# Kernel tuning notes

Measured on AMD Instinct MI355X. Metric: run time of the kernel, lower is better.

Reference implementation:

```python
import jax, jax.numpy as jnp
import numpy as np

C = 256
GROUPS = 8
EPS = 1e-5

def group_norm(x, gamma, beta):
    # x: [B, C, L]
    B, Cc, L = x.shape
    xg = x.reshape(B, GROUPS, Cc // GROUPS, L)
    mu = xg.mean(axis=(2, 3), keepdims=True)
    var = xg.var(axis=(2, 3), keepdims=True)
    xn = (xg - mu) / jnp.sqrt(var + EPS)
    xn = xn.reshape(B, Cc, L)
    return xn * gamma[None, :, None] + beta[None, :, None]

def conv1x1(x, W, b):
    # W: [Cout, Cin], x: [B, Cin, L]
    return jnp.einsum('oc,bcl->bol', W, x) + b[None, :, None]

def setup_inputs() -> dict:
    key = jax.random.key(0)
    ks = jax.random.split(key, 11)
    s = 1.0 / np.sqrt(C)
    inp = {
        'x': jax.random.normal(ks[0], (8, C, 2048), dtype=jnp.float32),
        'gamma': jnp.ones((C,), jnp.float32),
        'beta': jnp.zeros((C,), jnp.float32),
        'Wq': jax.random.uniform(ks[1], (C, C), jnp.float32, -s, s),
        'bq': jax.random.uniform(ks[2], (C,), jnp.float32, -s, s),
        'Wk': jax.random.uniform(ks[3], (C, C), jnp.float32, -s, s),
        'bk': jax.random.uniform(ks[4], (C,), jnp.float32, -s, s),
        'Wv': jax.random.uniform(ks[5], (C, C), jnp.float32, -s, s),
        'bv': jax.random.uniform(ks[6], (C,), jnp.float32, -s, s),
        'Wo': jax.random.uniform(ks[7], (C, C), jnp.float32, -s, s),
        'bo': jax.random.uniform(ks[8], (C,), jnp.float32, -s, s),
    }
    return inp

def reference(x, gamma, beta, Wq, bq, Wk, bk, Wv, bv, Wo, bo):
    h = group_norm(x, gamma, beta)
    q = conv1x1(h, Wq, bq)  # [B, C, L]
    k = conv1x1(h, Wk, bk)
    v = conv1x1(h, Wv, bv)
    scale = x.shape[1] ** (-0.5)
    attn = jnp.einsum('bci,bcj->bij', q, k) * scale  # [B, L, L]
    attn = jax.nn.softmax(attn, axis=-1)
    out = jnp.einsum('bij,bcj->bci', attn, v)  # [B, C, L]
    out = conv1x1(out, Wo, bo)
    return x + out
```

## Files before the change

kernel.cpp:

```cpp
#include <hip/hip_runtime.h>
#include <hip/hip_bf16.h>
#include <stddef.h>

#define NB 8
#define NC 256
#define NL 2048

typedef __attribute__((ext_vector_type(8))) short s16x8;
typedef __attribute__((ext_vector_type(4))) float f32x4;

__device__ __forceinline__ short f2bs(float x){
  __hip_bfloat16 h = __float2bfloat16(x);
  return __builtin_bit_cast(short, h);
}
__device__ __forceinline__ float bs2f(short x){
  unsigned u = ((unsigned)(unsigned short)x) << 16;
  return __builtin_bit_cast(float, u);
}

#define MFMA16(a,b,c) __builtin_amdgcn_mfma_f32_16x16x32_bf16((a),(b),(c),0,0,0)

__global__ __launch_bounds__(256) void k_stats_prep(const float* __restrict__ x, float* __restrict__ gpart,
                                                    const float* __restrict__ wq, const float* __restrict__ wk,
                                                    const float* __restrict__ wv, const float* __restrict__ wo,
                                                    short* __restrict__ wout){
  const int t = threadIdx.x;
  if (blockIdx.x >= 512){
    int idx = (blockIdx.x - 512) * 256 + t;
    int which = idx >> 16;
    int off = idx & 65535;
    const float* src = (which == 0) ? wq : (which == 1) ? wk : (which == 2) ? wv : wo;
    float sc = (which == 0) ? 0.0625f : 1.0f;
    wout[idx] = f2bs(src[off] * sc);
    return;
  }
  const int idx = blockIdx.x;
  const float4* base = (const float4*)(x + (size_t)idx * 8192);
  float s = 0.f, ss = 0.f;
  for (int i = t; i < 2048; i += 256){
    float4 v = base[i];
    s  += v.x + v.y + v.z + v.w;
    ss += v.x*v.x + v.y*v.y + v.z*v.z + v.w*v.w;
  }
  #pragma unroll
  for (int m = 32; m; m >>= 1){ s += __shfl_down(s, m); ss += __shfl_down(ss, m); }
  __shared__ float red[8];
  if ((t & 63) == 0){ red[t >> 6] = s; red[4 + (t >> 6)] = ss; }
  __syncthreads();
  if (t == 0){
    gpart[idx * 2 + 0] = red[0] + red[1] + red[2] + red[3];
    gpart[idx * 2 + 1] = red[4] + red[5] + red[6] + red[7];
  }
}

__global__ __launch_bounds__(256) void k_gapply(const float* __restrict__ x, const float* __restrict__ gamma,
                                                const float* __restrict__ beta, const float* __restrict__ gpart,
                                                short* __restrict__ ht){
  const int idx = blockIdx.x;
  const int bg = idx >> 3, lt8 = idx & 7;
  const int b = bg >> 3, g = bg & 7;
  float S = 0.f, SS = 0.f;
  #pragma unroll
  for (int s2 = 0; s2 < 8; ++s2){ S += gpart[(bg * 8 + s2) * 2]; SS += gpart[(bg * 8 + s2) * 2 + 1]; }
  const float mu = S * (1.f / 65536.f);
  const float var = SS * (1.f / 65536.f) - mu * mu;
  const float rstd = rsqrtf(var + 1e-5f);
  const float* xg = x + (size_t)bg * 65536;
  const int t = threadIdx.x;
  const int cc = t >> 3, lch = t & 7;
  const int c = g * 32 + cc;
  const float gsc = gamma[c] * rstd;
  const float gbi = beta[c] - mu * gsc;
  __shared__ short tile[64 * 33];
  const int ll_s = t & 63, cg = t >> 6;
  for (int lt = 0; lt < 4; ++lt){
    const int l0 = lt8 * 256 + lt * 64;
    const float4* rp = (const float4*)(xg + (size_t)cc * NL + l0 + lch * 8);
    float4 a = rp[0], bv = rp[1];
    float vals[8] = {a.x, a.y, a.z, a.w, bv.x, bv.y, bv.z, bv.w};
    short o[8];
    #pragma unroll
    for (int e = 0; e < 8; ++e) o[e] = f2bs(vals[e] * gsc + gbi);
    __syncthreads();
    #pragma unroll
    for (int e = 0; e < 8; ++e) tile[(lch * 8 + e) * 33 + cc] = o[e];
    __syncthreads();
    s16x8 pk;
    #pragma unroll
    for (int e = 0; e < 8; ++e) pk[e] = tile[ll_s * 33 + cg * 8 + e];
    *(s16x8*)(ht + ((size_t)(b * NL) + l0 + ll_s) * NC + g * 32 + cg * 8) = pk;
  }
}

__global__ __launch_bounds__(256) void k_conv_qkv(const short* __restrict__ ht, const short* __restrict__ wbf,
                                                  const float* __restrict__ bq, const float* __restrict__ bk,
                                                  const float* __restrict__ bv,
                                                  short* __restrict__ qt, short* __restrict__ kt,
                                                  short* __restrict__ vt){
  const int z = blockIdx.z;
  const int b = z & 7, which = z >> 3;
  const int lane = threadIdx.x & 63, wid = threadIdx.x >> 6;
  const int wr = wid >> 1, wc = wid & 1;
  const int kgrp = (lane >> 4) * 8;
  const short* aptr;
  const short* bptr;
  int m0, n0;
  if (which < 2){
    m0 = blockIdx.y * 128 + wr * 64;
    n0 = blockIdx.x * 64 + wc * 32;
    aptr = ht + ((size_t)(b * NL) + m0 + (lane & 15)) * NC + kgrp;
    bptr = wbf + (which ? 65536 : 0) + (size_t)(n0 + (lane & 15)) * NC + kgrp;
  } else {
    const int idx = blockIdx.y * 4 + blockIdx.x;
    m0 = (idx >> 5) * 128 + wr * 64;
    n0 = (idx & 31) * 64 + wc * 32;
    aptr = wbf + 2 * 65536 + (size_t)(m0 + (lane & 15)) * NC + kgrp;
    bptr = ht + ((size_t)(b * NL) + n0 + (lane & 15)) * NC + kgrp;
  }
  f32x4 acc[4][2];
  #pragma unroll
  for (int i = 0; i < 4; ++i){
    #pragma unroll
    for (int j = 0; j < 2; ++j){ f32x4 z2 = {0.f,0.f,0.f,0.f}; acc[i][j] = z2; }
  }
  #pragma unroll 2
  for (int kk = 0; kk < 256; kk += 32){
    s16x8 af[4], bfr[2];
    #pragma unroll
    for (int mf = 0; mf < 4; ++mf) af[mf] = *(const s16x8*)(aptr + (size_t)(mf * 16) * NC + kk);
    #pragma unroll
    for (int nf = 0; nf < 2; ++nf) bfr[nf] = *(const s16x8*)(bptr + (size_t)(nf * 16) * NC + kk);
    #pragma unroll
    for (int mf = 0; mf < 4; ++mf)
      #pragma unroll
      for (int nf = 0; nf < 2; ++nf)
        acc[mf][nf] = MFMA16(af[mf], bfr[nf], acc[mf][nf]);
  }
  if (which < 2){
    const float* bias = which ? bk : bq;
    const float bsc = which ? 1.0f : 0.0625f;
    short* outp = which ? kt : qt;
    #pragma unroll
    for (int nf = 0; nf < 2; ++nf){
      const int oc = n0 + nf * 16 + (lane & 15);
      const float bb = bias[oc] * bsc;
      #pragma unroll
      for (int mf = 0; mf < 4; ++mf){
        #pragma unroll
        for (int r = 0; r < 4; ++r){
          const int lr = m0 + mf * 16 + (lane >> 4) * 4 + r;
          outp[((size_t)(b * NL) + lr) * NC + oc] = f2bs(acc[mf][nf][r] + bb);
        }
      }
    }
  } else {
    #pragma unroll
    for (int mf = 0; mf < 4; ++mf){
      #pragma unroll
      for (int r = 0; r < 4; ++r){
        const int orow = m0 + mf * 16 + (lane >> 4) * 4 + r;
        const float bb = bv[orow];
        #pragma unroll
        for (int nf = 0; nf < 2; ++nf){
          const int lcol = n0 + nf * 16 + (lane & 15);
          vt[((size_t)(b * NC) + orow) * NL + lcol] = f2bs(acc[mf][nf][r] + bb);
        }
      }
    }
  }
}

__global__ __launch_bounds__(256, 2) void k_flash(const short* __restrict__ qt, const short* __restrict__ kt,
                                                  const short* __restrict__ v, short* __restrict__ po,
                                                  float* __restrict__ ml){
  const int flat = blockIdx.x;
  const int b = flat & 7;
  const int rest = flat >> 3;
  const int h = rest & 1;
  const int i0 = (rest >> 1) * 64;
  const int lane = threadIdx.x & 63, wid = threadIdx.x >> 6;
  __shared__ short k_lds[64 * 256];
  __shared__ short v_lds[256 * 64];
  __shared__ short plds[4][1024];
  short* pl = plds[wid];
  const int arow = lane & 15, kg = lane >> 4;

  const short* qp = qt + ((size_t)(b * NL) + i0 + wid * 16 + arow) * NC + kg * 8;
  s16x8 qf[8];
  #pragma unroll
  for (int kc = 0; kc < 8; ++kc) qf[kc] = *(const s16x8*)(qp + kc * 32);

  f32x4 oacc[16];
  #pragma unroll
  for (int i = 0; i < 16; ++i){ f32x4 z = {0.f,0.f,0.f,0.f}; oacc[i] = z; }
  float m_r[4], l_r[4];
  #pragma unroll
  for (int r = 0; r < 4; ++r){ m_r[r] = -3.0e38f; l_r[r] = 0.f; }

  auto STAGE_K = [&](int jt){
    const int j0 = jt * 64;
    #pragma unroll
    for (int t = 0; t < 8; ++t){
      const int i = wid * 8 + t;
      const int r = 2 * i + (lane >> 5);
      const int wb = (lane & 31) * 16;
      const short* src = kt + ((size_t)(b * NL) + j0 + r) * NC + ((wb ^ ((r & 15) << 4)) >> 1);
      __builtin_amdgcn_global_load_lds((const __attribute__((address_space(1))) void*)src,
                                       (__attribute__((address_space(3))) void*)&k_lds[i * 512], 16, 0, 0);
    }
  };
  auto STAGE_V = [&](int jt){
    const int j0 = jt * 64;
    #pragma unroll
    for (int t = 0; t < 8; ++t){
      const int i = wid * 8 + t;
      const int rc = 8 * i + (lane >> 3);
      const int wb = (lane & 7) * 16;
      const short* src = v + ((size_t)(b * NC) + rc) * NL + j0 + ((wb ^ ((rc & 7) << 4)) >> 1);
      __builtin_amdgcn_global_load_lds((const __attribute__((address_space(1))) void*)src,
                                       (__attribute__((address_space(3))) void*)&v_lds[i * 512], 16, 0, 0);
    }
  };

  const int jb0 = h * 16, jend = jb0 + 16;
  STAGE_K(jb0);
  STAGE_V(jb0);
  asm volatile("s_waitcnt vmcnt(0)" ::: "memory");
  __builtin_amdgcn_s_barrier();
  __builtin_amdgcn_sched_barrier(0);

  for (int jt = jb0; jt < jend; ++jt){
    f32x4 sf[4];
    #pragma unroll
    for (int nf = 0; nf < 4; ++nf){ f32x4 z = {0.f,0.f,0.f,0.f}; sf[nf] = z; }
    __builtin_amdgcn_s_setprio(1);
    #pragma unroll
    for (int kc = 0; kc < 8; ++kc){
      #pragma unroll
      for (int nf = 0; nf < 4; ++nf){
        const int r = nf * 16 + arow;
        s16x8 kf = *(const s16x8*)&k_lds[r * 256 + (((kc * 64 + kg * 16) ^ ((arow & 15) << 4)) >> 1)];
        sf[nf] = MFMA16(qf[kc], kf, sf[nf]);
      }
    }
    __builtin_amdgcn_s_setprio(0);
    float mx[4];
    #pragma unroll
    for (int r = 0; r < 4; ++r){
      float m2 = fmaxf(fmaxf(sf[0][r], sf[1][r]), fmaxf(sf[2][r], sf[3][r]));
      #pragma unroll
      for (int d = 1; d < 16; d <<= 1) m2 = fmaxf(m2, __shfl_xor(m2, d));
      mx[r] = m2;
    }
    const int ok = (mx[0] <= m_r[0] + 8.f) & (mx[1] <= m_r[1] + 8.f) &
                   (mx[2] <= m_r[2] + 8.f) & (mx[3] <= m_r[3] + 8.f);
    if (!__all(ok)){
      float corr[4];
      #pragma unroll
      for (int r = 0; r < 4; ++r){
        const float mn = fmaxf(m_r[r], mx[r]);
        corr[r] = __expf(m_r[r] - mn);
        m_r[r] = mn;
        l_r[r] *= corr[r];
      }
      #pragma unroll
      for (int i = 0; i < 16; ++i){
        f32x4 t = oacc[i];
        t[0] *= corr[0]; t[1] *= corr[1]; t[2] *= corr[2]; t[3] *= corr[3];
        oacc[i] = t;
      }
    }
    #pragma unroll
    for (int r = 0; r < 4; ++r){
      float rs = 0.f;
      #pragma unroll
      for (int nf = 0; nf < 4; ++nf){
        float p = __expf(sf[nf][r] - m_r[r]);
        sf[nf][r] = p;
        rs += p;
      }
      #pragma unroll
      for (int d = 1; d < 16; d <<= 1) rs += __shfl_xor(rs, d);
      l_r[r] += rs;
    }
    asm volatile("s_waitcnt vmcnt(0)" ::: "memory");
    __builtin_amdgcn_s_barrier();
    __builtin_amdgcn_sched_barrier(0);
    if (jt + 1 < jend) STAGE_K(jt + 1);

    #pragma unroll
    for (int r = 0; r < 4; ++r){
      const int rowp = kg * 4 + r;
      const int swz = (rowp & 7) << 3;
      #pragma unroll
      for (int nf = 0; nf < 4; ++nf){
        const int col = nf * 16 + arow;
        pl[rowp * 64 + (col ^ swz)] = f2bs(sf[nf][r]);
      }
    }
    __builtin_amdgcn_s_setprio(1);
    #pragma unroll
    for (int kc2 = 0; kc2 < 2; ++kc2){
      const int swz2 = (arow & 7) << 3;
      s16x8 pa = *(const s16x8*)(pl + arow * 64 + ((kc2 * 32 + kg * 8) ^ swz2));
      #pragma unroll
      for (int nf2 = 0; nf2 < 16; ++nf2){
        const int rc = nf2 * 16 + arow;
        s16x8 vf = *(const s16x8*)&v_lds[rc * 64 + (((kc2 * 64 + kg * 16) ^ ((rc & 7) << 4)) >> 1)];
        oacc[nf2] = MFMA16(pa, vf, oacc[nf2]);
      }
    }
    __builtin_amdgcn_s_setprio(0);
    __builtin_amdgcn_s_barrier();
    __builtin_amdgcn_sched_barrier(0);
    if (jt + 1 < jend) STAGE_V(jt + 1);
    asm volatile("s_waitcnt vmcnt(8)" ::: "memory");
    __builtin_amdgcn_s_barrier();
    __builtin_amdgcn_sched_barrier(0);
  }

  short* pob = po + (size_t)h * 4194304 + ((size_t)(b * NL) + i0 + wid * 16) * NC;
  #pragma unroll
  for (int r = 0; r < 4; ++r){
    const int irow = kg * 4 + r;
    #pragma unroll
    for (int nf2 = 0; nf2 < 16; ++nf2){
      pob[(size_t)irow * NC + nf2 * 16 + arow] = f2bs(oacc[nf2][r]);
    }
    if (arow == 0){
      const size_t Rg = (size_t)h * 16384 + (size_t)(b * NL) + i0 + wid * 16 + irow;
      ml[Rg * 2 + 0] = m_r[r];
      ml[Rg * 2 + 1] = l_r[r];
    }
  }
}

__global__ __launch_bounds__(256) void k_final(const short* __restrict__ po, const float* __restrict__ ml,
                                               const short* __restrict__ wo, const float* __restrict__ bo,
                                               const float* __restrict__ x, float* __restrict__ out){
  const int b = blockIdx.z;
  const int lane = threadIdx.x & 63, wid = threadIdx.x >> 6;
  const int wr = wid >> 1, wc = wid & 1;
  const int o0 = blockIdx.y * 128 + wr * 64;
  const int i0 = blockIdx.x * 64 + wc * 32;
  const int kgrp = (lane >> 4) * 8;
  const short* aptr = wo + (size_t)(o0 + (lane & 15)) * NC + kgrp;
  float wgt[2][2], winv[2];
  size_t rbase[2];
  #pragma unroll
  for (int nf = 0; nf < 2; ++nf){
    const int Rg = b * NL + i0 + nf * 16 + (lane & 15);
    rbase[nf] = (size_t)Rg * NC + kgrp;
    const float m0 = ml[(size_t)Rg * 2],             l0 = ml[(size_t)Rg * 2 + 1];
    const float m1 = ml[((size_t)16384 + Rg) * 2],   l1 = ml[((size_t)16384 + Rg) * 2 + 1];
    const float mm = fmaxf(m0, m1);
    wgt[nf][0] = __expf(m0 - mm);
    wgt[nf][1] = __expf(m1 - mm);
    winv[nf] = 1.f / (l0 * wgt[nf][0] + l1 * wgt[nf][1]);
  }
  f32x4 acc[4][2];
  #pragma unroll
  for (int i = 0; i < 4; ++i){
    #pragma unroll
    for (int j = 0; j < 2; ++j){ f32x4 z = {0.f,0.f,0.f,0.f}; acc[i][j] = z; }
  }
  for (int kk = 0; kk < 256; kk += 32){
    s16x8 af[4], bfr[2];
    #pragma unroll
    for (int mf = 0; mf < 4; ++mf) af[mf] = *(const s16x8*)(aptr + (size_t)(mf * 16) * NC + kk);
    #pragma unroll
    for (int nf = 0; nf < 2; ++nf){
      s16x8 p0 = *(const s16x8*)(po + rbase[nf] + kk);
      s16x8 p1 = *(const s16x8*)(po + (size_t)4194304 + rbase[nf] + kk);
      #pragma unroll
      for (int e = 0; e < 8; ++e)
        bfr[nf][e] = f2bs((wgt[nf][0] * bs2f(p0[e]) + wgt[nf][1] * bs2f(p1[e])) * winv[nf]);
    }
    #pragma unroll
    for (int mf = 0; mf < 4; ++mf)
      #pragma unroll
      for (int nf = 0; nf < 2; ++nf)
        acc[mf][nf] = MFMA16(af[mf], bfr[nf], acc[mf][nf]);
  }
  #pragma unroll
  for (int mf = 0; mf < 4; ++mf){
    #pragma unroll
    for (int r = 0; r < 4; ++r){
      const int orow = o0 + mf * 16 + (lane >> 4) * 4 + r;
      const float bb = bo[orow];
      #pragma unroll
      for (int nf = 0; nf < 2; ++nf){
        const int icol = i0 + nf * 16 + (lane & 15);
        const size_t idx = ((size_t)(b * NC) + orow) * NL + icol;
        out[idx] = acc[mf][nf][r] + bb + x[idx];
      }
    }
  }
}

extern "C" void kernel_launch(void* const* d_in, const int* in_sizes, int n_in,
                              void* d_out, int out_size, void* d_ws, size_t ws_size,
                              hipStream_t stream){
  const float* x     = (const float*)d_in[0];
  const float* gamma = (const float*)d_in[1];
  const float* beta  = (const float*)d_in[2];
  const float* Wq    = (const float*)d_in[3];
  const float* bq    = (const float*)d_in[4];
  const float* Wk    = (const float*)d_in[5];
  const float* bk    = (const float*)d_in[6];
  const float* Wv    = (const float*)d_in[7];
  const float* bv    = (const float*)d_in[8];
  const float* Wo    = (const float*)d_in[9];
  const float* bo    = (const float*)d_in[10];
  float* out = (float*)d_out;

  char* ws = (char*)d_ws;
  short* wbf = (short*)ws;
  short* ht  = (short*)(ws + (size_t)524288);
  short* qt  = (short*)(ws + (size_t)524288 + 8388608);
  short* ktp = (short*)(ws + (size_t)524288 + 2 * 8388608);
  short* vp  = (short*)(ws + (size_t)524288 + 3 * 8388608);
  short* pop = (short*)(ws + (size_t)524288 + 4 * 8388608);
  float* mlp = (float*)(ws + (size_t)524288 + 6 * 8388608);
  float* gpp = (float*)(ws + (size_t)524288 + 6 * 8388608 + 262144);

  k_stats_prep<<<1536, 256, 0, stream>>>(x, gpp, Wq, Wk, Wv, Wo, wbf);
  k_gapply<<<512, 256, 0, stream>>>(x, gamma, beta, gpp, ht);
  k_conv_qkv<<<dim3(4, 16, 24), 256, 0, stream>>>(ht, wbf, bq, bk, bv, qt, ktp, vp);
  k_flash  <<<dim3(512), 256, 0, stream>>>(qt, ktp, vp, pop, mlp);
  k_final  <<<dim3(32, 2, 8), 256, 0, stream>>>(pop, mlp, wbf + 3 * 65536, bo, x, out);
}
```

Baseline: 133.1 us.

## Double-buffer K tiles in LDS and read V fragments directly from global

The flash attention kernel drops the V staging buffer and instead has each wave load its V MFMA operands straight from global memory into registers. K tiles are double-buffered in LDS, so the next tile's prefetch is issued at the top of each iteration and only one barrier per iteration remains. This cuts LDS traffic and synchronisation. In exchange, all four waves redundantly fetch the same V data from global/L2, and P·V now waits on global load latency instead of LDS.

```diff
diff --git a/kernel.cpp b/kernel.cpp
--- a/kernel.cpp
+++ b/kernel.cpp
@@ -179,8 +179,7 @@
   const int h = rest & 1;
   const int i0 = (rest >> 1) * 64;
   const int lane = threadIdx.x & 63, wid = threadIdx.x >> 6;
-  __shared__ short k_lds[64 * 256];
-  __shared__ short v_lds[256 * 64];
+  __shared__ short k_lds[2][64 * 256];
   __shared__ short plds[4][1024];
   short* pl = plds[wid];
   const int arow = lane & 15, kg = lane >> 4;
@@ -189,6 +188,7 @@
   s16x8 qf[8];
   #pragma unroll
   for (int kc = 0; kc < 8; ++kc) qf[kc] = *(const s16x8*)(qp + kc * 32);
+  const short* vbase = v + ((size_t)(b * NC) + arow) * NL + kg * 8;
 
   f32x4 oacc[16];
   #pragma unroll
@@ -197,7 +197,7 @@
   #pragma unroll
   for (int r = 0; r < 4; ++r){ m_r[r] = -3.0e38f; l_r[r] = 0.f; }
 
-  auto STAGE_K = [&](int jt){
+  auto STAGE_K = [&](int jt, int buf){
     const int j0 = jt * 64;
     #pragma unroll
     for (int t = 0; t < 8; ++t){
@@ -206,30 +206,21 @@
       const int wb = (lane & 31) * 16;
       const short* src = kt + ((size_t)(b * NL) + j0 + r) * NC + ((wb ^ ((r & 15) << 4)) >> 1);
       __builtin_amdgcn_global_load_lds((const __attribute__((address_space(1))) void*)src,
-                                       (__attribute__((address_space(3))) void*)&k_lds[i * 512], 16, 0, 0);
+                                       (__attribute__((address_space(3))) void*)&k_lds[buf][i * 512], 16, 0, 0);
     }
   };
-  auto STAGE_V = [&](int jt){
-    const int j0 = jt * 64;
-    #pragma unroll
-    for (int t = 0; t < 8; ++t){
-      const int i = wid * 8 + t;
-      const int rc = 8 * i + (lane >> 3);
-      const int wb = (lane & 7) * 16;
-      const short* src = v + ((size_t)(b * NC) + rc) * NL + j0 + ((wb ^ ((rc & 7) << 4)) >> 1);
-      __builtin_amdgcn_global_load_lds((const __attribute__((address_space(1))) void*)src,
-                                       (__attribute__((address_space(3))) void*)&v_lds[i * 512], 16, 0, 0);
-    }
-  };
 
   const int jb0 = h * 16, jend = jb0 + 16;
-  STAGE_K(jb0);
-  STAGE_V(jb0);
+  STAGE_K(jb0, 0);
   asm volatile("s_waitcnt vmcnt(0)" ::: "memory");
   __builtin_amdgcn_s_barrier();
   __builtin_amdgcn_sched_barrier(0);
 
+  int cur = 0;
   for (int jt = jb0; jt < jend; ++jt){
+    const int j0 = jt * 64;
+    if (jt + 1 < jend) STAGE_K(jt + 1, cur ^ 1);
+    const short* kl = k_lds[cur];
     f32x4 sf[4];
     #pragma unroll
     for (int nf = 0; nf < 4; ++nf){ f32x4 z = {0.f,0.f,0.f,0.f}; sf[nf] = z; }
@@ -239,7 +230,7 @@
       #pragma unroll
       for (int nf = 0; nf < 4; ++nf){
         const int r = nf * 16 + arow;
-        s16x8 kf = *(const s16x8*)&k_lds[r * 256 + (((kc * 64 + kg * 16) ^ ((arow & 15) << 4)) >> 1)];
+        s16x8 kf = *(const s16x8*)&kl[r * 256 + (((kc * 64 + kg * 16) ^ ((arow & 15) << 4)) >> 1)];
         sf[nf] = MFMA16(qf[kc], kf, sf[nf]);
       }
     }
@@ -283,40 +274,37 @@
       for (int d = 1; d < 16; d <<= 1) rs += __shfl_xor(rs, d);
       l_r[r] += rs;
     }
+    #pragma unroll
+    for (int r = 0; r < 4; ++r){
+      const int rowp = kg * 4 + r;
+      const int swz = (rowp & 7) << 3;
+      #pragma unroll
+      for (int nf = 0; nf < 4; ++nf){
+        const int col = nf * 16 + arow;
+        pl[rowp * 64 + (col ^ swz)] = f2bs(sf[nf][r]);
+      }
+    }
+    __builtin_amdgcn_s_setprio(1);
+    #pragma unroll
+    for (int kc2 = 0; kc2 < 2; ++kc2){
+      const int swz2 = (arow & 7) << 3;
+      s16x8 pa = *(const s16x8*)(pl + arow * 64 + ((kc2 * 32 + kg * 8) ^ swz2));
+      #pragma unroll
+      for (int half = 0; half < 2; ++half){
+        s16x8 vfa[8];
+        #pragma unroll
+        for (int g = 0; g < 8; ++g)
+          vfa[g] = *(const s16x8*)(vbase + (size_t)((half * 8 + g) * 16) * NL + j0 + kc2 * 32);
+        #pragma unroll
+        for (int g = 0; g < 8; ++g)
+          oacc[half * 8 + g] = MFMA16(pa, vfa[g], oacc[half * 8 + g]);
+      }
+    }
+    __builtin_amdgcn_s_setprio(0);
     asm volatile("s_waitcnt vmcnt(0)" ::: "memory");
     __builtin_amdgcn_s_barrier();
     __builtin_amdgcn_sched_barrier(0);
-    if (jt + 1 < jend) STAGE_K(jt + 1);
-
-    #pragma unroll
-    for (int r = 0; r < 4; ++r){
-      const int rowp = kg * 4 + r;
-      const int swz = (rowp & 7) << 3;
-      #pragma unroll
-      for (int nf = 0; nf < 4; ++nf){
-        const int col = nf * 16 + arow;
-        pl[rowp * 64 + (col ^ swz)] = f2bs(sf[nf][r]);
-      }
-    }
-    __builtin_amdgcn_s_setprio(1);
-    #pragma unroll
-    for (int kc2 = 0; kc2 < 2; ++kc2){
-      const int swz2 = (arow & 7) << 3;
-      s16x8 pa = *(const s16x8*)(pl + arow * 64 + ((kc2 * 32 + kg * 8) ^ swz2));
-      #pragma unroll
-      for (int nf2 = 0; nf2 < 16; ++nf2){
-        const int rc = nf2 * 16 + arow;
-        s16x8 vf = *(const s16x8*)&v_lds[rc * 64 + (((kc2 * 64 + kg * 16) ^ ((rc & 7) << 4)) >> 1)];
-        oacc[nf2] = MFMA16(pa, vf, oacc[nf2]);
-      }
-    }
-    __builtin_amdgcn_s_setprio(0);
-    __builtin_amdgcn_s_barrier();
-    __builtin_amdgcn_sched_barrier(0);
-    if (jt + 1 < jend) STAGE_V(jt + 1);
-    asm volatile("s_waitcnt vmcnt(8)" ::: "memory");
-    __builtin_amdgcn_s_barrier();
-    __builtin_amdgcn_sched_barrier(0);
+    cur ^= 1;
   }
 
   short* pob = po + (size_t)h * 4194304 + ((size_t)(b * NL) + i0 + wid * 16) * NC;
```

Result: slower. 224.3 us (+68.5%).
